# Kernel optimization log

Measured on AMD Instinct MI355X. Metric: run time of the kernel, lower is better.

Reference implementation:

```python
import jax, jax.numpy as jnp
import numpy as np

N = 32768      # total atoms in batch
D_IN = 1024    # input feature dimension
H1 = 512       # encoder/decoder hidden width
LAT = 128      # latent dimension
D_OUT = 1024   # output dimension
E = 4          # number of unique element symbols (experts)


def _xavier(key, shape):
    # torch.nn.init.xavier_uniform_ on Linear weights
    fan_in, fan_out = shape[-2], shape[-1]
    limit = np.sqrt(6.0 / (fan_in + fan_out)).astype(np.float32)
    return jax.random.uniform(key, shape, jnp.float32, -limit, limit)


def setup_inputs() -> dict:
    key = jax.random.key(0)
    ks = jax.random.split(key, 8)
    X = jax.random.normal(ks[0], (N, D_IN), jnp.float32)
    sym_ids = jax.random.randint(ks[1], (N,), 0, E)
    # stacked per-symbol (expert) weights: topology 1024->512->128->512->1024
    We1 = _xavier(ks[2], (E, D_IN, H1));  be1 = jnp.zeros((E, H1), jnp.float32)
    We2 = _xavier(ks[3], (E, H1, LAT));   be2 = jnp.zeros((E, LAT), jnp.float32)
    Wd1 = _xavier(ks[4], (E, LAT, H1));   bd1 = jnp.zeros((E, H1), jnp.float32)
    Wd2 = _xavier(ks[5], (E, H1, D_OUT)); bd2 = jnp.zeros((E, D_OUT), jnp.float32)
    return {"X": X, "sym_ids": sym_ids,
            "We1": We1, "be1": be1, "We2": We2, "be2": be2,
            "Wd1": Wd1, "bd1": bd1, "Wd2": Wd2, "bd2": bd2}


def reference(X, sym_ids, We1, be1, We2, be2, Wd1, bd1, Wd2, bd2):
    # Dense MoE-style dispatch: compute every expert on the full batch (E is
    # tiny and fixed), then select each atom's own-symbol output. Same math as
    # the per-atom Python-loop routing in the original forward.
    def expert(e):
        h = jax.nn.relu(X @ We1[e] + be1[e])          # [N, H1]  encoder layer 1
        z = jax.nn.relu(h @ We2[e] + be2[e])          # [N, LAT] latent (encoder layer 2)
        d = jax.nn.relu(z @ Wd1[e] + bd1[e])          # [N, H1]  decoder layer 1
        return d @ Wd2[e] + bd2[e]                    # [N, D_OUT] final Linear, no activation

    outs = jnp.stack([expert(e) for e in range(E)])   # [E, N, D_OUT]
    # route: pick expert sym_ids[n] for atom n
    return jnp.take_along_axis(outs, sym_ids[None, :, None], axis=0)[0]
```

## Files before the change

kernel.cpp:

```cpp
#include <hip/hip_runtime.h>
#include <hip/hip_bf16.h>
#include <stdint.h>

typedef __bf16 bf16x8 __attribute__((ext_vector_type(8)));
typedef float  f32x4  __attribute__((ext_vector_type(4)));

#define NATOMS  32768
#define NEXP    4
#define MAXROWS (NATOMS + NEXP*256)
#define MB256   (MAXROWS/256)
#define MB128   (MAXROWS/128)
#define MGRP    ((MB256 + 7)/8)
#define XCONV   2048

#define WS_HDR   0u
#define WS_PERM  1024u
#define WS_W1T   136192u
#define WS_W2T   (WS_W1T + 4194304u)
#define WS_W3T   (WS_W2T + 524288u)
#define WS_W4T   (WS_W3T + 524288u)
#define WS_H     (WS_W4T + 4194304u)
#define WS_D     WS_H
#define WS_XB    (WS_H + 34603008u)

__device__ __forceinline__ unsigned short f2bf(float f){
  union { float f; uint32_t u; } v; v.f = f;
  uint32_t r = v.u + 0x7fffu + ((v.u >> 16) & 1u);
  return (unsigned short)(r >> 16);
}
__device__ __forceinline__ uint32_t pk2(float a, float b){
  return (uint32_t)f2bf(a) | ((uint32_t)f2bf(b) << 16);
}
__device__ __forceinline__ void glds16(const void* g, void* l){
  __builtin_amdgcn_global_load_lds(
      (const __attribute__((address_space(1))) uint32_t*)g,
      (__attribute__((address_space(3))) uint32_t*)l, 16, 0, 0);
}

template<int K, int NO>
__device__ __forceinline__ void wtile1024(const float* __restrict__ W,
                                          unsigned short* __restrict__ Bt,
                                          int b, unsigned short (*tile)[65]){
  const int nx = NO/64, ny = K/64;
  const int e = b / (nx*ny), rem = b % (nx*ny);
  const int k0 = (rem / nx) * 64;
  const int n0 = (rem % nx) * 64;
  const int t  = threadIdx.x;
  const int c  = t & 63;
  const float* Wb = W + ((size_t)e*K + k0)*NO + n0;
  #pragma unroll
  for (int i=0;i<4;++i){
    int r = (t>>6) + i*16;
    tile[r][c] = f2bf(Wb[(size_t)r*NO + c]);
  }
  __syncthreads();
  unsigned short* Bb = Bt + ((size_t)e*NO + n0)*K + k0;
  #pragma unroll
  for (int i=0;i<4;++i){
    int r = (t>>6) + i*16;
    Bb[(size_t)r*K + c] = tile[c][r];
  }
}

__global__ __launch_bounds__(1024) void prep_kernel(
    const int*   __restrict__ sym,  int* __restrict__ hdr,  int* __restrict__ perm,
    const float* __restrict__ X,    unsigned short* __restrict__ Xb,
    const float* __restrict__ We1, unsigned short* __restrict__ W1t,
    const float* __restrict__ We2, unsigned short* __restrict__ W2t,
    const float* __restrict__ Wd1, unsigned short* __restrict__ W3t,
    const float* __restrict__ Wd2, unsigned short* __restrict__ W4t)
{
  __shared__ unsigned short tile[64][65];
  __shared__ unsigned wsumA[16], wsumB[16];
  __shared__ unsigned wexclA[16], wexclB[16];
  __shared__ int pof[NEXP+1];
  __shared__ int tot[NEXP];

  int b = blockIdx.x;
  const int t = threadIdx.x;

  if (b == 0){
    const int lane = t & 63, w = t >> 6;
    int c0=0,c1=0,c2=0,c3=0;
    const int base = t*32;
    for (int i=0;i<32;++i){
      int s = sym[base+i];
      c0 += (s==0); c1 += (s==1); c2 += (s==2); c3 += (s==3);
    }
    unsigned pA = (unsigned)c0 | ((unsigned)c1<<16);
    unsigned pB = (unsigned)c2 | ((unsigned)c3<<16);
    unsigned iA = pA, iB = pB;
    #pragma unroll
    for (int d=1; d<64; d<<=1){
      unsigned uA = __shfl_up(iA, d, 64);
      unsigned uB = __shfl_up(iB, d, 64);
      if (lane >= d){ iA += uA; iB += uB; }
    }
    unsigned exA = iA - pA, exB = iB - pB;
    if (lane == 63){ wsumA[w] = iA; wsumB[w] = iB; }
    __syncthreads();
    if (w == 0 && lane < 16){
      unsigned vA = wsumA[lane], vB = wsumB[lane];
      unsigned jA = vA, jB = vB;
      #pragma unroll
      for (int d=1; d<16; d<<=1){
        unsigned uA = __shfl_up(jA, d, 64);
        unsigned uB = __shfl_up(jB, d, 64);
        if (lane >= d){ jA += uA; jB += uB; }
      }
      wexclA[lane] = jA - vA; wexclB[lane] = jB - vB;
      if (lane == 15){
        tot[0] = (int)(jA & 0xFFFFu); tot[1] = (int)(jA >> 16);
        tot[2] = (int)(jB & 0xFFFFu); tot[3] = (int)(jB >> 16);
        int o = 0; pof[0] = 0;
        for (int e=0;e<NEXP;++e){ o += (tot[e]+255)&~255; pof[e+1]=o; }
        for (int e=0;e<=NEXP;++e) hdr[e]=pof[e];
      }
    }
    __syncthreads();
    const unsigned bA = wexclA[w] + exA, bB = wexclB[w] + exB;
    int p0 = pof[0] + (int)(bA & 0xFFFFu);
    int p1 = pof[1] + (int)(bA >> 16);
    int p2 = pof[2] + (int)(bB & 0xFFFFu);
    int p3 = pof[3] + (int)(bB >> 16);
    for (int i=t; i<MAXROWS; i+=1024) perm[i] = -1;
    __syncthreads();
    for (int i=0;i<32;++i){
      int a = base+i; int s = sym[a];
      if      (s==0) perm[p0++] = a;
      else if (s==1) perm[p1++] = a;
      else if (s==2) perm[p2++] = a;
      else           perm[p3++] = a;
    }
    return;
  }
  b -= 1;
  if (b < XCONV){
    size_t i = ((size_t)b*1024 + t) * 16;
    const float4* src = (const float4*)(X + i);
    float4 f0 = src[0], f1 = src[1], f2 = src[2], f3 = src[3];
    uint4 o0, o1;
    o0.x = pk2(f0.x,f0.y); o0.y = pk2(f0.z,f0.w);
    o0.z = pk2(f1.x,f1.y); o0.w = pk2(f1.z,f1.w);
    o1.x = pk2(f2.x,f2.y); o1.y = pk2(f2.z,f2.w);
    o1.z = pk2(f3.x,f3.y); o1.w = pk2(f3.z,f3.w);
    *(uint4*)&Xb[i]     = o0;
    *(uint4*)&Xb[i + 8] = o1;
    return;
  }
  b -= XCONV;
  if (b < 512){ wtile1024<1024, 512>(We1, W1t, b, tile); return; }
  b -= 512;
  if (b <  64){ wtile1024< 512, 128>(We2, W2t, b, tile); return; }
  b -= 64;
  if (b <  64){ wtile1024< 128, 512>(Wd1, W3t, b, tile); return; }
  b -= 64;
  wtile1024< 512,1024>(Wd2, W4t, b, tile);
}

template<int K, int NO, int NT, bool RELU, bool GATHER, bool FINAL>
__global__ __launch_bounds__(512, 4) void gemm_big(
    const unsigned short* __restrict__ A,
    const unsigned short* __restrict__ Bt,
    const float* __restrict__ bias,
    unsigned short* __restrict__ Cb,
    float* __restrict__ Cf,
    const int* __restrict__ hdr,
    const int* __restrict__ perm)
{
  __shared__ __align__(16) unsigned short smem[256*64 + 128*64];
  __shared__ int sperm[256];
  unsigned short* As = smem;
  unsigned short* Bs = smem + 256*64;

  const int b = blockIdx.x;
  const int grp = b / (8*NT), rem = b % (8*NT);
  const int rowblk = grp*8 + (rem & 7);
  const int row0 = rowblk * 256;
  if (row0 >= hdr[NEXP]) return;
  const int ntile = rem >> 3;
  const int e = (row0 >= hdr[1]) + (row0 >= hdr[2]) + (row0 >= hdr[3]);
  const int n0 = ntile * 128;

  const int t = threadIdx.x;
  const int lane = t & 63, wid = t >> 6;

  if constexpr (GATHER || FINAL){
    if (t < 256) sperm[t] = perm[row0 + t];
    __syncthreads();
  }

  const int l8 = lane >> 3;
  const int scoff = (((lane & 7) ^ l8) << 3);

  const unsigned short* asrc[4];
  #pragma unroll
  for (int i=0;i<4;++i){
    const int r = wid*32 + i*8 + l8;
    long grow;
    if constexpr (GATHER){
      int a = sperm[r];
      grow = (a < 0) ? 0 : a;
    } else {
      grow = row0 + r;
    }
    asrc[i] = A + (size_t)grow*K + scoff;
  }
  const unsigned short* bsrc[2];
  #pragma unroll
  for (int i=0;i<2;++i)
    bsrc[i] = Bt + ((size_t)e*NO + n0 + wid*16 + i*8 + l8)*K + scoff;

  const int lr   = lane & 15;
  const int sgrp = lane >> 4;
  const int wr   = (wid >> 1) * 64;
  const int wc   = (wid & 1) * 64;

  f32x4 acc[4][4];
  const f32x4 z4 = {0.f,0.f,0.f,0.f};
  #pragma unroll
  for (int mi=0;mi<4;++mi)
    #pragma unroll
    for (int ni=0;ni<4;++ni) acc[mi][ni] = z4;

  #pragma unroll 1
  for (int kt = 0; kt < K/64; ++kt){
    __syncthreads();
    #pragma unroll
    for (int i=0;i<4;++i)
      glds16(asrc[i] + kt*64, As + (wid*4+i)*512);
    #pragma unroll
    for (int i=0;i<2;++i)
      glds16(bsrc[i] + kt*64, Bs + (wid*2+i)*512);
    __syncthreads();

    #pragma unroll
    for (int kk=0;kk<2;++kk){
      bf16x8 af[4], bfr[4];
      const int s = kk*4 + sgrp;
      #pragma unroll
      for (int mi=0;mi<4;++mi){
        int R = wr + mi*16 + lr;
        af[mi] = *(const bf16x8*)&As[R*64 + ((s ^ (R & 7)) << 3)];
      }
      #pragma unroll
      for (int ni=0;ni<4;++ni){
        int Cc = wc + ni*16 + lr;
        bfr[ni] = *(const bf16x8*)&Bs[Cc*64 + ((s ^ (Cc & 7)) << 3)];
      }
      #pragma unroll
      for (int mi=0;mi<4;++mi)
        #pragma unroll
        for (int ni=0;ni<4;++ni)
          acc[mi][ni] = __builtin_amdgcn_mfma_f32_16x16x32_bf16(af[mi], bfr[ni], acc[mi][ni], 0, 0, 0);
    }
  }

  __syncthreads();
  if constexpr (FINAL){
    float* stf = (float*)smem;
    #pragma unroll
    for (int qr=0; qr<4; ++qr){
      if ((wid >> 1) == qr){
        #pragma unroll
        for (int ni=0;ni<4;++ni){
          const int colg = n0 + wc + ni*16 + lr;
          const float bv_ = bias[(size_t)e*NO + colg];
          #pragma unroll
          for (int mi=0;mi<4;++mi){
            #pragma unroll
            for (int q=0;q<4;++q){
              float v = acc[mi][ni][q] + bv_;
              if (RELU) v = fmaxf(v, 0.f);
              stf[(mi*16 + sgrp*4 + q)*132 + wc + ni*16 + lr] = v;
            }
          }
        }
      }
      __syncthreads();
      #pragma unroll
      for (int i=0;i<4;++i){
        int idx = t + 512*i;
        int r = idx >> 5, c4 = idx & 31;
        int atom = sperm[qr*64 + r];
        if (atom >= 0)
          *(float4*)&Cf[(size_t)atom*NO + n0 + c4*4] = *(const float4*)&stf[r*132 + c4*4];
      }
      __syncthreads();
    }
  } else {
    unsigned short* st = smem;
    const int wrl = ((wid >> 1) & 1) * 64;
    #pragma unroll
    for (int h=0; h<2; ++h){
      if ((wid >> 2) == h){
        #pragma unroll
        for (int ni=0;ni<4;++ni){
          const int colg = n0 + wc + ni*16 + lr;
          const float bv_ = bias[(size_t)e*NO + colg];
          #pragma unroll
          for (int mi=0;mi<4;++mi){
            #pragma unroll
            for (int q=0;q<4;++q){
              float v = acc[mi][ni][q] + bv_;
              if (RELU) v = fmaxf(v, 0.f);
              st[(wrl + mi*16 + sgrp*4 + q)*136 + wc + ni*16 + lr] = f2bf(v);
            }
          }
        }
      }
      __syncthreads();
      #pragma unroll
      for (int i=0;i<4;++i){
        int idx = t + 512*i;
        int r = idx >> 4, c8 = idx & 15;
        *(uint4*)&Cb[(size_t)(row0 + h*128 + r)*NO + n0 + c8*8] = *(const uint4*)&st[r*136 + c8*8];
      }
      __syncthreads();
    }
  }
}

__global__ __launch_bounds__(256, 2) void fused_mid(
    const unsigned short* H,
    const unsigned short* __restrict__ W2,
    const float* __restrict__ b2,
    const unsigned short* __restrict__ W3,
    const float* __restrict__ b3,
    unsigned short* D,
    const int* __restrict__ hdr)
{
  __shared__ __align__(16) unsigned short un[128*136];
  __shared__ __align__(16) unsigned short Zs[128*128];
  unsigned short* As = un;
  unsigned short* Bs = un + 128*64;

  const int row0 = blockIdx.x * 128;
  if (row0 >= hdr[NEXP]) return;
  const int e = (row0 >= hdr[1]) + (row0 >= hdr[2]) + (row0 >= hdr[3]);

  const int t = threadIdx.x;
  const int lane = t & 63, wid = t >> 6;
  const int l8 = lane >> 3;
  const int scoff = (((lane & 7) ^ l8) << 3);
  const int lr = lane & 15, sgrp = lane >> 4;
  const int wr = (wid >> 1) * 64, wc = (wid & 1) * 64;

  const unsigned short* asrc[4];
  const unsigned short* bsrc[4];
  #pragma unroll
  for (int i=0;i<4;++i){
    asrc[i] = H  + (size_t)(row0 + wid*32 + i*8 + l8)*512 + scoff;
    bsrc[i] = W2 + ((size_t)e*128 + wid*32 + i*8 + l8)*512 + scoff;
  }

  f32x4 acc[4][4];
  const f32x4 z4 = {0.f,0.f,0.f,0.f};
  #pragma unroll
  for (int mi=0;mi<4;++mi)
    #pragma unroll
    for (int ni=0;ni<4;++ni) acc[mi][ni] = z4;

  #pragma unroll 1
  for (int kt = 0; kt < 8; ++kt){
    __syncthreads();
    #pragma unroll
    for (int i=0;i<4;++i){
      glds16(asrc[i] + kt*64, As + (wid*4+i)*512);
      glds16(bsrc[i] + kt*64, Bs + (wid*4+i)*512);
    }
    __syncthreads();
    #pragma unroll
    for (int kk=0;kk<2;++kk){
      bf16x8 af[4], bfr[4];
      const int s = kk*4 + sgrp;
      #pragma unroll
      for (int mi=0;mi<4;++mi){
        int R = wr + mi*16 + lr;
        af[mi] = *(const bf16x8*)&As[R*64 + ((s ^ (R & 7)) << 3)];
      }
      #pragma unroll
      for (int ni=0;ni<4;++ni){
        int Cc = wc + ni*16 + lr;
        bfr[ni] = *(const bf16x8*)&Bs[Cc*64 + ((s ^ (Cc & 7)) << 3)];
      }
      #pragma unroll
      for (int mi=0;mi<4;++mi)
        #pragma unroll
        for (int ni=0;ni<4;++ni)
          acc[mi][ni] = __builtin_amdgcn_mfma_f32_16x16x32_bf16(af[mi], bfr[ni], acc[mi][ni], 0, 0, 0);
    }
  }
  #pragma unroll
  for (int ni=0;ni<4;++ni){
    const int col = wc + ni*16 + lr;
    const float bv_ = b2[(size_t)e*128 + col];
    const int ch = col >> 3, cl = col & 7;
    #pragma unroll
    for (int mi=0;mi<4;++mi){
      #pragma unroll
      for (int q=0;q<4;++q){
        const int row = wr + mi*16 + sgrp*4 + q;
        float v = fmaxf(acc[mi][ni][q] + bv_, 0.f);
        Zs[row*128 + ((ch ^ (row & 15)) << 3) + cl] = f2bf(v);
      }
    }
  }
  __syncthreads();

  bf16x8 afk[4][4];
  #pragma unroll
  for (int kk=0;kk<4;++kk)
    #pragma unroll
    for (int mi=0;mi<4;++mi){
      int R = wr + mi*16 + lr;
      afk[kk][mi] = *(const bf16x8*)&Zs[R*128 + (((kk*4+sgrp) ^ (R & 15)) << 3)];
    }

  #pragma unroll 1
  for (int nt=0; nt<4; ++nt){
    #pragma unroll
    for (int i=0;i<8;++i){
      int R = (wid*8 + i)*4 + (lane >> 4);
      int sch = (lane & 15) ^ (R & 15);
      glds16(W3 + ((size_t)e*512 + nt*128 + R)*128 + sch*8, un + (size_t)(wid*8+i)*512);
    }
    __syncthreads();

    #pragma unroll
    for (int mi=0;mi<4;++mi)
      #pragma unroll
      for (int ni=0;ni<4;++ni) acc[mi][ni] = z4;

    #pragma unroll
    for (int kk=0;kk<4;++kk){
      bf16x8 bfr[4];
      const int s = kk*4 + sgrp;
      #pragma unroll
      for (int ni=0;ni<4;++ni){
        int Cc = wc + ni*16 + lr;
        bfr[ni] = *(const bf16x8*)&un[Cc*128 + ((s ^ (Cc & 15)) << 3)];
      }
      #pragma unroll
      for (int mi=0;mi<4;++mi)
        #pragma unroll
        for (int ni=0;ni<4;++ni)
          acc[mi][ni] = __builtin_amdgcn_mfma_f32_16x16x32_bf16(afk[kk][mi], bfr[ni], acc[mi][ni], 0, 0, 0);
    }
    __syncthreads();

    #pragma unroll
    for (int ni=0;ni<4;++ni){
      const int col = wc + ni*16 + lr;
      const float bv_ = b3[(size_t)e*512 + nt*128 + col];
      #pragma unroll
      for (int mi=0;mi<4;++mi){
        #pragma unroll
        for (int q=0;q<4;++q){
          const int row = wr + mi*16 + sgrp*4 + q;
          float v = fmaxf(acc[mi][ni][q] + bv_, 0.f);
          un[row*136 + col] = f2bf(v);
        }
      }
    }
    __syncthreads();
    #pragma unroll
    for (int i=0;i<8;++i){
      int idx = t + 256*i;
      int r = idx >> 4, c8 = idx & 15;
      *(uint4*)&D[(size_t)(row0 + r)*512 + nt*128 + c8*8] = *(const uint4*)&un[r*136 + c8*8];
    }
    __syncthreads();
  }
}

extern "C" void kernel_launch(void* const* d_in, const int* in_sizes, int n_in,
                              void* d_out, int out_size, void* d_ws, size_t ws_size,
                              hipStream_t stream) {
  const float* X   = (const float*)d_in[0];
  const int*   sym = (const int*)  d_in[1];
  const float* We1 = (const float*)d_in[2];
  const float* be1 = (const float*)d_in[3];
  const float* We2 = (const float*)d_in[4];
  const float* be2 = (const float*)d_in[5];
  const float* Wd1 = (const float*)d_in[6];
  const float* bd1 = (const float*)d_in[7];
  const float* Wd2 = (const float*)d_in[8];
  const float* bd2 = (const float*)d_in[9];
  float* out = (float*)d_out;

  char* ws = (char*)d_ws;
  int* hdr  = (int*)(ws + WS_HDR);
  int* perm = (int*)(ws + WS_PERM);
  unsigned short* W1t = (unsigned short*)(ws + WS_W1T);
  unsigned short* W2t = (unsigned short*)(ws + WS_W2T);
  unsigned short* W3t = (unsigned short*)(ws + WS_W3T);
  unsigned short* W4t = (unsigned short*)(ws + WS_W4T);
  unsigned short* H   = (unsigned short*)(ws + WS_H);
  unsigned short* Dd  = (unsigned short*)(ws + WS_D);
  unsigned short* Xb  = (unsigned short*)(ws + WS_XB);

  dim3 b256(256), b512(512), b1024(1024);
  prep_kernel<<<dim3(1 + XCONV + 512 + 64 + 64 + 512), b1024, 0, stream>>>(
      sym, hdr, perm, X, Xb, We1, W1t, We2, W2t, Wd1, W3t, Wd2, W4t);

  gemm_big<1024, 512, 4, true,  true,  false><<<dim3(MGRP*8*4), b512, 0, stream>>>(
      Xb, W1t, be1, H, nullptr, hdr, perm);
  fused_mid<<<dim3(MB128), b256, 0, stream>>>(H, W2t, be2, W3t, bd1, Dd, hdr);
  gemm_big< 512,1024, 8, false, false, true ><<<dim3(MGRP*8*8), b512, 0, stream>>>(
      Dd, W4t, bd2, nullptr, out, hdr, perm);
}
```

Measured before the change: 205.6 us.

## Parallelize atom routing with per-block histograms and ballot-based scatter

Replaces the single-block serial count/scan/scatter of atoms by expert with a three-stage scheme. A 128-block histogram kernel is followed by a one-block prefix kernel computing per-256-atom-chunk base offsets, and 32 prep blocks then scatter using wave ballots and popcounts. This removes a long serial tail from one 1024-thread block inside prep_kernel, at the cost of two extra small kernel launches with their launch latency.

Result: faster. 197.4 us (-4.0%).

```diff
diff --git a/kernel.cpp b/kernel.cpp
--- a/kernel.cpp
+++ b/kernel.cpp
@@ -12,10 +12,13 @@
 #define MB128   (MAXROWS/128)
 #define MGRP    ((MB256 + 7)/8)
 #define XCONV   2048
+#define SCAT    32
 
 #define WS_HDR   0u
 #define WS_PERM  1024u
-#define WS_W1T   136192u
+#define WS_BC    136192u
+#define WS_BB    138240u
+#define WS_W1T   140288u
 #define WS_W2T   (WS_W1T + 4194304u)
 #define WS_W3T   (WS_W2T + 524288u)
 #define WS_W4T   (WS_W3T + 524288u)
@@ -35,6 +38,43 @@
   __builtin_amdgcn_global_load_lds(
       (const __attribute__((address_space(1))) uint32_t*)g,
       (__attribute__((address_space(3))) uint32_t*)l, 16, 0, 0);
+}
+
+__global__ __launch_bounds__(256) void routeA(const int* __restrict__ sym,
+                                              int* __restrict__ bc,
+                                              int* __restrict__ perm){
+  __shared__ int h[NEXP];
+  const int t = threadIdx.x, b = blockIdx.x;
+  if (t < NEXP) h[t] = 0;
+  for (int i = b*256 + t; i < MAXROWS; i += 128*256) perm[i] = -1;
+  __syncthreads();
+  int s = sym[b*256 + t];
+  atomicAdd(&h[s], 1);
+  __syncthreads();
+  if (t < NEXP) bc[b*NEXP + t] = h[t];
+}
+
+__global__ __launch_bounds__(64) void routeB(const int* __restrict__ bc,
+                                             int* __restrict__ hdr,
+                                             int* __restrict__ bb){
+  __shared__ int tot[NEXP], pof[NEXP+1];
+  const int t = threadIdx.x;
+  if (t < NEXP){
+    int s = 0;
+    for (int i=0;i<128;++i) s += bc[i*NEXP + t];
+    tot[t] = s;
+  }
+  __syncthreads();
+  if (t == 0){
+    int o = 0; pof[0] = 0;
+    for (int e=0;e<NEXP;++e){ o += (tot[e]+255)&~255; pof[e+1]=o; }
+    for (int e=0;e<=NEXP;++e) hdr[e]=pof[e];
+  }
+  __syncthreads();
+  if (t < NEXP){
+    int run = pof[t];
+    for (int i=0;i<128;++i){ bb[i*NEXP + t] = run; run += bc[i*NEXP + t]; }
+  }
 }
 
 template<int K, int NO>
@@ -63,7 +103,7 @@
 }
 
 __global__ __launch_bounds__(1024) void prep_kernel(
-    const int*   __restrict__ sym,  int* __restrict__ hdr,  int* __restrict__ perm,
+    const int*   __restrict__ sym,  const int* __restrict__ bb,  int* __restrict__ perm,
     const float* __restrict__ X,    unsigned short* __restrict__ Xb,
     const float* __restrict__ We1, unsigned short* __restrict__ W1t,
     const float* __restrict__ We2, unsigned short* __restrict__ W2t,
@@ -71,70 +111,37 @@
     const float* __restrict__ Wd2, unsigned short* __restrict__ W4t)
 {
   __shared__ unsigned short tile[64][65];
-  __shared__ unsigned wsumA[16], wsumB[16];
-  __shared__ unsigned wexclA[16], wexclB[16];
-  __shared__ int pof[NEXP+1];
-  __shared__ int tot[NEXP];
+  __shared__ int wc[16][NEXP];
 
   int b = blockIdx.x;
   const int t = threadIdx.x;
 
-  if (b == 0){
+  if (b < SCAT){
     const int lane = t & 63, w = t >> 6;
-    int c0=0,c1=0,c2=0,c3=0;
-    const int base = t*32;
-    for (int i=0;i<32;++i){
-      int s = sym[base+i];
-      c0 += (s==0); c1 += (s==1); c2 += (s==2); c3 += (s==3);
-    }
-    unsigned pA = (unsigned)c0 | ((unsigned)c1<<16);
-    unsigned pB = (unsigned)c2 | ((unsigned)c3<<16);
-    unsigned iA = pA, iB = pB;
-    #pragma unroll
-    for (int d=1; d<64; d<<=1){
-      unsigned uA = __shfl_up(iA, d, 64);
-      unsigned uB = __shfl_up(iB, d, 64);
-      if (lane >= d){ iA += uA; iB += uB; }
-    }
-    unsigned exA = iA - pA, exB = iB - pB;
-    if (lane == 63){ wsumA[w] = iA; wsumB[w] = iB; }
-    __syncthreads();
-    if (w == 0 && lane < 16){
-      unsigned vA = wsumA[lane], vB = wsumB[lane];
-      unsigned jA = vA, jB = vB;
-      #pragma unroll
-      for (int d=1; d<16; d<<=1){
-        unsigned uA = __shfl_up(jA, d, 64);
-        unsigned uB = __shfl_up(jB, d, 64);
-        if (lane >= d){ jA += uA; jB += uB; }
-      }
-      wexclA[lane] = jA - vA; wexclB[lane] = jB - vB;
-      if (lane == 15){
-        tot[0] = (int)(jA & 0xFFFFu); tot[1] = (int)(jA >> 16);
-        tot[2] = (int)(jB & 0xFFFFu); tot[3] = (int)(jB >> 16);
-        int o = 0; pof[0] = 0;
-        for (int e=0;e<NEXP;++e){ o += (tot[e]+255)&~255; pof[e+1]=o; }
-        for (int e=0;e<=NEXP;++e) hdr[e]=pof[e];
-      }
-    }
-    __syncthreads();
-    const unsigned bA = wexclA[w] + exA, bB = wexclB[w] + exB;
-    int p0 = pof[0] + (int)(bA & 0xFFFFu);
-    int p1 = pof[1] + (int)(bA >> 16);
-    int p2 = pof[2] + (int)(bB & 0xFFFFu);
-    int p3 = pof[3] + (int)(bB >> 16);
-    for (int i=t; i<MAXROWS; i+=1024) perm[i] = -1;
-    __syncthreads();
-    for (int i=0;i<32;++i){
-      int a = base+i; int s = sym[a];
-      if      (s==0) perm[p0++] = a;
-      else if (s==1) perm[p1++] = a;
-      else if (s==2) perm[p2++] = a;
-      else           perm[p3++] = a;
-    }
+    const int a = b*1024 + t;
+    const int s = sym[a];
+    unsigned long long b0 = __ballot(s & 1);
+    unsigned long long b1 = __ballot(s & 2);
+    unsigned long long meq = ((s & 1) ? b0 : ~b0) & ((s & 2) ? b1 : ~b1);
+    unsigned long long lt  = ((unsigned long long)1 << lane) - 1;
+    const int lofs = __popcll(meq & lt);
+    if (lane == 0){
+      unsigned long long m00 = ~b0 & ~b1, m01 = b0 & ~b1, m10 = ~b0 & b1, m11 = b0 & b1;
+      wc[w][0] = __popcll(m00); wc[w][1] = __popcll(m01);
+      wc[w][2] = __popcll(m10); wc[w][3] = __popcll(m11);
+    }
+    __syncthreads();
+    int wbase = 0;
+    for (int i=0;i<w;++i) wbase += wc[i][s];
+    const int rb = (t >> 8);
+    int wbase_rb = 0;
+    for (int i = rb*4; i < w; ++i) wbase_rb += wc[i][s];
+    const int slot = bb[(b*4 + rb)*NEXP + s] + wbase_rb + lofs;
+    perm[slot] = a;
+    (void)wbase;
     return;
   }
-  b -= 1;
+  b -= SCAT;
   if (b < XCONV){
     size_t i = ((size_t)b*1024 + t) * 16;
     const float4* src = (const float4*)(X + i);
@@ -492,6 +499,8 @@
   char* ws = (char*)d_ws;
   int* hdr  = (int*)(ws + WS_HDR);
   int* perm = (int*)(ws + WS_PERM);
+  int* bc   = (int*)(ws + WS_BC);
+  int* bb   = (int*)(ws + WS_BB);
   unsigned short* W1t = (unsigned short*)(ws + WS_W1T);
   unsigned short* W2t = (unsigned short*)(ws + WS_W2T);
   unsigned short* W3t = (unsigned short*)(ws + WS_W3T);
@@ -501,8 +510,10 @@
   unsigned short* Xb  = (unsigned short*)(ws + WS_XB);
 
   dim3 b256(256), b512(512), b1024(1024);
-  prep_kernel<<<dim3(1 + XCONV + 512 + 64 + 64 + 512), b1024, 0, stream>>>(
-      sym, hdr, perm, X, Xb, We1, W1t, We2, W2t, Wd1, W3t, Wd2, W4t);
+  routeA<<<dim3(128), b256, 0, stream>>>(sym, bc, perm);
+  routeB<<<dim3(1), dim3(64), 0, stream>>>(bc, hdr, bb);
+  prep_kernel<<<dim3(SCAT + XCONV + 512 + 64 + 64 + 512), b1024, 0, stream>>>(
+      sym, bb, perm, X, Xb, We1, W1t, We2, W2t, Wd1, W3t, Wd2, W4t);
 
   gemm_big<1024, 512, 4, true,  true,  false><<<dim3(MGRP*8*4), b512, 0, stream>>>(
       Xb, W1t, be1, H, nullptr, hdr, perm);
```
